# Kernel optimization log

Measured on AMD Instinct MI355X. Metric: run time of the kernel, lower is better.

## Reference

```python
import jax, jax.numpy as jnp
import numpy as np

N_NODES = 50000
N_EDGES = 800000
IN_C = 128
OUT_C = 128
ALPHA = 0.2  # leaky_relu negative slope (args.egat_alpha)
EDGE_K = 3   # edgefeat width, fixed by W_out in-dim = 3*out_channels


def setup_inputs() -> dict:
    key = jax.random.key(0)
    k = jax.random.split(key, 7)
    h = jax.random.normal(k[0], (N_NODES, IN_C), dtype=jnp.float32)
    edge_index = jax.random.randint(k[1], (2, N_EDGES), 0, N_NODES, dtype=jnp.int64)
    edgefeat = jax.random.uniform(k[2], (N_EDGES, EDGE_K), dtype=jnp.float32)
    # glorot-initialized linear weights (stored as [in, out] for x @ W)
    def glorot(kk, fan_in, fan_out):
        lim = jnp.sqrt(6.0 / (fan_in + fan_out)).astype(jnp.float32)
        return jax.random.uniform(kk, (fan_in, fan_out), jnp.float32, -lim, lim)
    W = glorot(k[3], IN_C, OUT_C)
    a1 = glorot(k[4], OUT_C, 1)
    a2 = glorot(k[5], OUT_C, 1)
    W_out = glorot(k[6], EDGE_K * OUT_C, OUT_C)
    return {"h": h, "edge_index": edge_index, "edgefeat": edgefeat,
            "W": W, "a1": a1, "a2": a2, "W_out": W_out}


def reference(h, edge_index, edgefeat, W, a1, a2, W_out):
    src = edge_index[0]  # j: message source
    dst = edge_index[1]  # i: aggregation target
    n = h.shape[0]

    Wh = h @ W                                   # [N, C]
    s1 = Wh @ a1                                 # [N, 1] alpha_j scores
    s2 = Wh @ a2                                 # [N, 1] alpha_i scores

    # edge_update: leaky_relu(alpha_j + alpha_i) * edge_attr, then edge softmax over dst
    e = s1[src] + s2[dst]                        # [E, 1]
    e = jnp.where(e >= 0, e, ALPHA * e)
    alpha = e * edgefeat                         # [E, 3]
    m = jax.ops.segment_max(alpha, dst, num_segments=n)      # [N, 3]
    m = jnp.where(jnp.isfinite(m), m, 0.0)
    ex = jnp.exp(alpha - m[dst])
    denom = jax.ops.segment_sum(ex, dst, num_segments=n)     # [N, 3]
    att = ex / (denom[dst] + 1e-16)              # [E, 3] (dropout p applied at eval -> identity)

    # message: outer product att[E,3] x x_j[E,C] -> [E, 3C] -> W_out -> [E, C]
    x_j = Wh[src]                                # [E, C]
    msg = (att[:, :, None] * x_j[:, None, :]).reshape(att.shape[0], EDGE_K * Wh.shape[1])
    msg = msg @ W_out                            # [E, C]

    # aggregate: sum at destination nodes
    out = jax.ops.segment_sum(msg, dst, num_segments=n)      # [N, C]
    return out
```

## Files before the change

### kernel.cpp

```cpp
#include <hip/hip_runtime.h>
#include <hip/hip_bf16.h>

#define ALPHA 0.2f
typedef unsigned int uint32;
typedef __attribute__((ext_vector_type(8))) short short8;
typedef __attribute__((ext_vector_type(4))) float f32x4;

static __device__ __forceinline__ unsigned short f2bf(float f) {
    unsigned int u = __float_as_uint(f);
    u += 0x7fffu + ((u >> 16) & 1u);
    return (unsigned short)(u >> 16);
}
static __device__ __forceinline__ uint32 pk2bf(float lo, float hi) {
    return (uint32)f2bf(lo) | ((uint32)f2bf(hi) << 16);
}
static __device__ __forceinline__ float bflo(uint32 u) { return __uint_as_float(u << 16); }
static __device__ __forceinline__ float bfhi(uint32 u) { return __uint_as_float(u & 0xffff0000u); }

__global__ __launch_bounds__(256) void k1_hist_prep(const int* __restrict__ ei,
                                                    int* __restrict__ counts,
                                                    int* __restrict__ eslot, int E,
                                                    const float* __restrict__ W,
                                                    const float* __restrict__ Wout,
                                                    const float* __restrict__ a1,
                                                    const float* __restrict__ a2,
                                                    unsigned short* __restrict__ WBT,
                                                    unsigned short* __restrict__ WoutT,
                                                    float* __restrict__ w1f,
                                                    float* __restrict__ w2f, int nbh) {
    const int tid = threadIdx.x;
    if ((int)blockIdx.x < nbh) {
        int e = blockIdx.x * 256 + tid;
        if (e < E) eslot[e] = atomicAdd(&counts[ei[E + e]], 1);
        return;
    }
    int bp = blockIdx.x - nbh;
    if (bp < 8) {
        for (int n = bp * 16; n < bp * 16 + 16; ++n)
            for (int c = tid; c < 128; c += 256)
                WBT[n * 128 + c] = f2bf(W[c * 128 + n]);
    } else if (bp < 24) {
        int q = bp - 8;
        for (int n = q * 8; n < q * 8 + 8; ++n)
            for (int c = tid; c < 384; c += 256)
                WoutT[n * 384 + c] = f2bf(Wout[c * 128 + n]);
    } else {
        if (tid < 128) {
            float acc1 = 0.f, acc2 = 0.f;
            for (int c = 0; c < 128; ++c) {
                float w = W[tid * 128 + c];
                acc1 += w * a1[c];
                acc2 += w * a2[c];
            }
            w1f[tid] = acc1;
            w2f[tid] = acc2;
        }
    }
}

__global__ __launch_bounds__(256) void k2_mmy_scan(const float* __restrict__ h,
                                                   const unsigned short* __restrict__ WBT,
                                                   const float* __restrict__ w1f,
                                                   const float* __restrict__ w2f,
                                                   unsigned short* __restrict__ Whb,
                                                   float* __restrict__ s1,
                                                   uint2* __restrict__ PR, int M,
                                                   const int* __restrict__ counts,
                                                   int* __restrict__ rowptr,
                                                   int N, int E, int nbm) {
    __shared__ unsigned short As[64 * 128];
    __shared__ unsigned short Bs[128 * 128];
    __shared__ float ws1[128], ws2[128];
    __shared__ int wsums[4];
    __shared__ int base_s;
    const int tid = threadIdx.x;

    if ((int)blockIdx.x >= nbm) {
        const int bs   = blockIdx.x - nbm;
        const int lane = tid & 63, wv = tid >> 6;
        const int limit = bs * 1024;
        int acc = 0;
        for (int i = tid * 4; i < limit; i += 1024) {
            int4 v = *(const int4*)(counts + i);
            acc += v.x + v.y + v.z + v.w;
        }
#pragma unroll
        for (int off = 32; off > 0; off >>= 1) acc += __shfl_down(acc, off);
        if (lane == 0) wsums[wv] = acc;
        __syncthreads();
        if (tid == 0) base_s = wsums[0] + wsums[1] + wsums[2] + wsums[3];
        __syncthreads();
        int i0 = bs * 1024 + tid * 4;
        int v0 = 0, v1 = 0, v2 = 0, v3 = 0;
        if (i0 + 3 < N) {
            int4 v = *(const int4*)(counts + i0);
            v0 = v.x; v1 = v.y; v2 = v.z; v3 = v.w;
        } else {
            if (i0 + 0 < N) v0 = counts[i0 + 0];
            if (i0 + 1 < N) v1 = counts[i0 + 1];
            if (i0 + 2 < N) v2 = counts[i0 + 2];
            if (i0 + 3 < N) v3 = counts[i0 + 3];
        }
        int tt = v0 + v1 + v2 + v3;
        int incl = tt;
#pragma unroll
        for (int off = 1; off < 64; off <<= 1) {
            int t = __shfl_up(incl, off);
            if (lane >= off) incl += t;
        }
        __syncthreads();
        if (lane == 63) wsums[wv] = incl;
        __syncthreads();
        int woff = 0;
        for (int w2 = 0; w2 < wv; ++w2) woff += wsums[w2];
        int base = base_s + woff + (incl - tt);
        if (i0 + 0 < N) { rowptr[i0 + 0] = base;                PR[i0 + 0].y = (uint32)base; }
        if (i0 + 1 < N) { rowptr[i0 + 1] = base + v0;           PR[i0 + 1].y = (uint32)(base + v0); }
        if (i0 + 2 < N) { rowptr[i0 + 2] = base + v0 + v1;      PR[i0 + 2].y = (uint32)(base + v0 + v1); }
        if (i0 + 3 < N) { rowptr[i0 + 3] = base + v0 + v1 + v2; PR[i0 + 3].y = (uint32)(base + v0 + v1 + v2); }
        if (bs == 0 && tid == 0) rowptr[N] = E;
        return;
    }

    const int lane = tid & 63;
    const int w    = tid >> 6;
    const int row0 = blockIdx.x * 64;

    if (tid < 128) ws1[tid] = w1f[tid];
    else           ws2[tid - 128] = w2f[tid - 128];
    __syncthreads();

    const float4* h4 = (const float4*)h;
    float sp1[4], sp2[4];
#pragma unroll
    for (int m = 0; m < 4; ++m) { sp1[m] = 0.f; sp2[m] = 0.f; }
#pragma unroll
    for (int m = 0; m < 4; ++m) {
        int i = m * 256 + tid;
        int r = i >> 4, g = i & 15;
        int rg = row0 + r;
        float4 va = make_float4(0.f, 0.f, 0.f, 0.f), vb = va;
        if (rg < M) {
            va = h4[(size_t)rg * 32 + g * 2];
            vb = h4[(size_t)rg * 32 + g * 2 + 1];
        }
        float4 wa1 = *(const float4*)(ws1 + g * 8);
        float4 wb1 = *(const float4*)(ws1 + g * 8 + 4);
        float4 wa2 = *(const float4*)(ws2 + g * 8);
        float4 wb2 = *(const float4*)(ws2 + g * 8 + 4);
        sp1[m] += va.x * wa1.x + va.y * wa1.y + va.z * wa1.z + va.w * wa1.w
                + vb.x * wb1.x + vb.y * wb1.y + vb.z * wb1.z + vb.w * wb1.w;
        sp2[m] += va.x * wa2.x + va.y * wa2.y + va.z * wa2.z + va.w * wa2.w
                + vb.x * wb2.x + vb.y * wb2.y + vb.z * wb2.z + vb.w * wb2.w;
        uint4 u;
        u.x = pk2bf(va.x, va.y); u.y = pk2bf(va.z, va.w);
        u.z = pk2bf(vb.x, vb.y); u.w = pk2bf(vb.z, vb.w);
        *(uint4*)(As + r * 128 + ((g ^ (r & 15)) * 8)) = u;
    }
#pragma unroll
    for (int m = 0; m < 4; ++m) {
#pragma unroll
        for (int off = 1; off < 16; off <<= 1) {
            sp1[m] += __shfl_xor(sp1[m], off);
            sp2[m] += __shfl_xor(sp2[m], off);
        }
    }
    if ((tid & 15) == 0) {
#pragma unroll
        for (int m = 0; m < 4; ++m) {
            int rg = row0 + m * 16 + (tid >> 4);
            if (rg < M) { s1[rg] = sp1[m]; PR[rg].x = __float_as_uint(sp2[m]); }
        }
    }

#pragma unroll
    for (int m = 0; m < 8; ++m) {
        int i = m * 256 + tid;
        int n = i >> 4, g = i & 15;
        uint4 v = *(const uint4*)(WBT + n * 128 + g * 8);
        *(uint4*)(Bs + n * 128 + ((g ^ (n & 15)) * 8)) = v;
    }
    __syncthreads();

    const int ml   = lane & 15;
    const int quad = lane >> 4;
    f32x4 acc[8];
#pragma unroll
    for (int nt = 0; nt < 8; ++nt) acc[nt] = (f32x4){0.f, 0.f, 0.f, 0.f};
#pragma unroll
    for (int kc = 0; kc < 4; ++kc) {
        int gl = ((kc * 4 + quad) ^ ml) * 8;
        short8 af = *(const short8*)(As + (w * 16 + ml) * 128 + gl);
#pragma unroll
        for (int nt = 0; nt < 8; ++nt) {
            short8 bf = *(const short8*)(Bs + (nt * 16 + ml) * 128 + gl);
            acc[nt] = __builtin_amdgcn_mfma_f32_16x16x32_bf16(af, bf, acc[nt], 0, 0, 0);
        }
    }
    __syncthreads();
    unsigned short* Ct = Bs;
    int lrow = w * 16 + quad * 4;
#pragma unroll
    for (int r = 0; r < 4; ++r)
#pragma unroll
        for (int nt = 0; nt < 8; ++nt)
            Ct[(lrow + r) * 136 + nt * 16 + ml] = f2bf(acc[nt][r]);
    __syncthreads();
#pragma unroll
    for (int m = 0; m < 4; ++m) {
        int i = m * 256 + tid;
        int r2 = i >> 4, g = i & 15;
        int rg = row0 + r2;
        uint4 v = *(const uint4*)(Ct + r2 * 136 + g * 8);
        if (rg < M)
            *(uint4*)(Whb + (size_t)rg * 128 + g * 8) = v;
    }
}

__global__ __launch_bounds__(256) void scatter_kernel(const int* __restrict__ ei,
                                                      const float* __restrict__ ef,
                                                      const float* __restrict__ s1,
                                                      const uint2* __restrict__ PR,
                                                      const int* __restrict__ eslot,
                                                      uint2* __restrict__ rec8, int E) {
    int e = blockIdx.x * blockDim.x + threadIdx.x;
    if (e >= E) return;
    int src = ei[e];
    int dst = ei[E + e];
    uint2 pr = PR[dst];
    float s = s1[src] + __uint_as_float(pr.x);
    s = (s >= 0.f) ? s : ALPHA * s;
    unsigned short b0 = f2bf(__expf(s * ef[e * 3 + 0]));
    unsigned short b1 = f2bf(__expf(s * ef[e * 3 + 1]));
    unsigned short b2 = f2bf(__expf(s * ef[e * 3 + 2]));
    uint2 rv;
    rv.x = (uint32)src | ((uint32)(b0 & 0x7fffu) << 17);
    rv.y = (uint32)(b1 & 0x7fffu) | ((uint32)(b2 & 0x7fffu) << 15);
    int pos = (int)pr.y + eslot[e];
    rec8[pos] = rv;
}

__global__ __launch_bounds__(1024) void agg_fused(const uint2* __restrict__ rec8,
                                                  const int* __restrict__ rowptr,
                                                  const uint32* __restrict__ Yu,
                                                  const unsigned short* __restrict__ WoutT,
                                                  float* __restrict__ out, int N) {
    __shared__ float CtS[2 * 16 * 132];
    uint32* zs32 = (uint32*)CtS;
    const int tid  = threadIdx.x;
    const int lane = tid & 63, w = tid >> 6;
    const int ml   = lane & 15, quad = lane >> 4;
    const int nb   = blockIdx.x * 16;
    const int node = nb + w;

    if (node < N) {
        int beg = rowptr[node], end = rowptr[node + 1];

        float d0 = 0.f, d1 = 0.f, d2 = 0.f;
        float z0l = 0.f, z0h = 0.f, z1l = 0.f, z1h = 0.f, z2l = 0.f, z2h = 0.f;
        int j = beg;
        for (; j + 7 < end; j += 8) {
            uint2 rr[8];
#pragma unroll
            for (int q = 0; q < 8; ++q) rr[q] = rec8[j + q];
            uint32 sx[8], sy[8];
#pragma unroll
            for (int q = 0; q < 8; ++q) {
                sx[q] = __builtin_amdgcn_readfirstlane(rr[q].x);
                sy[q] = __builtin_amdgcn_readfirstlane(rr[q].y);
            }
            uint32 u[8];
#pragma unroll
            for (int q = 0; q < 8; ++q)
                u[q] = Yu[(size_t)(sx[q] & 0x1ffffu) * 64 + lane];
#pragma unroll
            for (int q = 0; q < 8; ++q) {
                float w0 = __uint_as_float((sx[q] >> 1) & 0x7fff0000u);
                float w1 = __uint_as_float((sy[q] << 16) & 0x7fff0000u);
                float w2 = __uint_as_float((sy[q] << 1) & 0x7fff0000u);
                d0 += w0; d1 += w1; d2 += w2;
                float yl = bflo(u[q]), yh = bfhi(u[q]);
                z0l += w0 * yl; z0h += w0 * yh;
                z1l += w1 * yl; z1h += w1 * yh;
                z2l += w2 * yl; z2h += w2 * yh;
            }
        }
        for (; j + 3 < end; j += 4) {
            uint2 rr[4];
#pragma unroll
            for (int q = 0; q < 4; ++q) rr[q] = rec8[j + q];
            uint32 sx[4], sy[4];
#pragma unroll
            for (int q = 0; q < 4; ++q) {
                sx[q] = __builtin_amdgcn_readfirstlane(rr[q].x);
                sy[q] = __builtin_amdgcn_readfirstlane(rr[q].y);
            }
            uint32 u[4];
#pragma unroll
            for (int q = 0; q < 4; ++q)
                u[q] = Yu[(size_t)(sx[q] & 0x1ffffu) * 64 + lane];
#pragma unroll
            for (int q = 0; q < 4; ++q) {
                float w0 = __uint_as_float((sx[q] >> 1) & 0x7fff0000u);
                float w1 = __uint_as_float((sy[q] << 16) & 0x7fff0000u);
                float w2 = __uint_as_float((sy[q] << 1) & 0x7fff0000u);
                d0 += w0; d1 += w1; d2 += w2;
                float yl = bflo(u[q]), yh = bfhi(u[q]);
                z0l += w0 * yl; z0h += w0 * yh;
                z1l += w1 * yl; z1h += w1 * yh;
                z2l += w2 * yl; z2h += w2 * yh;
            }
        }
        for (; j < end; ++j) {
            uint2 r0 = rec8[j];
            uint32 sx = __builtin_amdgcn_readfirstlane(r0.x);
            uint32 sy = __builtin_amdgcn_readfirstlane(r0.y);
            uint32 u0 = Yu[(size_t)(sx & 0x1ffffu) * 64 + lane];
            float w0 = __uint_as_float((sx >> 1) & 0x7fff0000u);
            float w1 = __uint_as_float((sy << 16) & 0x7fff0000u);
            float w2 = __uint_as_float((sy << 1) & 0x7fff0000u);
            d0 += w0; d1 += w1; d2 += w2;
            float yl = bflo(u0), yh = bfhi(u0);
            z0l += w0 * yl; z0h += w0 * yh;
            z1l += w1 * yl; z1h += w1 * yh;
            z2l += w2 * yl; z2h += w2 * yh;
        }
        float i0 = 1.f / (d0 + 1e-16f);
        float i1 = 1.f / (d1 + 1e-16f);
        float i2 = 1.f / (d2 + 1e-16f);
        uint32 zp[3] = { pk2bf(z0l * i0, z0h * i0),
                         pk2bf(z1l * i1, z1h * i1),
                         pk2bf(z2l * i2, z2h * i2) };
#pragma unroll
        for (int k = 0; k < 3; ++k) {
            int g  = k * 16 + (lane >> 2);
            int sg = (g & ~7) | ((g ^ w) & 7);
            zs32[w * 192 + sg * 4 + (lane & 3)] = zp[k];
        }
    } else {
#pragma unroll
        for (int k = 0; k < 3; ++k)
            zs32[w * 192 + k * 64 + lane] = 0u;
    }
    __syncthreads();

    const int n0 = (w & 7) * 16;
    const int kh = w >> 3;
    f32x4 acc = (f32x4){0.f, 0.f, 0.f, 0.f};
    const unsigned short* zs16 = (const unsigned short*)zs32;
#pragma unroll
    for (int ks = 0; ks < 6; ++ks) {
        int g  = kh * 24 + ks * 4 + quad;
        int sg = (g & ~7) | ((g ^ ml) & 7);
        short8 af = *(const short8*)(zs16 + ml * 384 + sg * 8);
        short8 bf = *(const short8*)(WoutT + (size_t)(n0 + ml) * 384 + g * 8);
        acc = __builtin_amdgcn_mfma_f32_16x16x32_bf16(af, bf, acc, 0, 0, 0);
    }
    __syncthreads();
#pragma unroll
    for (int r = 0; r < 4; ++r)
        CtS[kh * 2112 + (quad * 4 + r) * 132 + n0 + ml] = acc[r];
    __syncthreads();
    if (tid < 512) {
        int row = tid >> 5, g = tid & 31;
        int nd  = nb + row;
        if (nd < N) {
            float4 a = *(const float4*)(CtS + row * 132 + g * 4);
            float4 b = *(const float4*)(CtS + 2112 + row * 132 + g * 4);
            *(float4*)(out + (size_t)nd * 128 + g * 4) =
                make_float4(a.x + b.x, a.y + b.y, a.z + b.z, a.w + b.w);
        }
    }
}

extern "C" void kernel_launch(void* const* d_in, const int* in_sizes, int n_in,
                              void* d_out, int out_size, void* d_ws, size_t ws_size,
                              hipStream_t stream) {
    const float* h    = (const float*)d_in[0];
    const int*   ei   = (const int*)d_in[1];
    const float* ef   = (const float*)d_in[2];
    const float* W    = (const float*)d_in[3];
    const float* a1   = (const float*)d_in[4];
    const float* a2   = (const float*)d_in[5];
    const float* Wout = (const float*)d_in[6];
    float*       out  = (float*)d_out;

    const int N = in_sizes[0] / 128;
    const int E = in_sizes[2] / 3;
    const int nchunk = (N + 1023) / 1024;
    const int nbh    = (E + 255) / 256;
    const int nbm    = (N + 63) / 64;

    uint2* rec8 = (uint2*)d_ws;
    unsigned short* Whb = (unsigned short*)(rec8 + E);
    unsigned short* WBT = Whb + (size_t)N * 128;
    unsigned short* WoutT = WBT + 128 * 128;
    float* w1f  = (float*)(WoutT + 128 * 384);
    float* w2f  = w1f + 128;
    float* s1   = w2f + 128;
    uint2* PR   = (uint2*)(s1 + N);
    int* rowptr = (int*)(PR + N);
    int* counts = rowptr + N + 4;
    int* eslot  = counts + N;

    (void)hipMemsetAsync(counts, 0, (size_t)N * sizeof(int), stream);

    k1_hist_prep<<<nbh + 25, 256, 0, stream>>>(ei, counts, eslot, E,
                                               W, Wout, a1, a2, WBT, WoutT, w1f, w2f, nbh);
    k2_mmy_scan<<<nbm + nchunk, 256, 0, stream>>>(h, WBT, w1f, w2f, Whb, s1, PR, N,
                                                  counts, rowptr, N, E, nbm);
    scatter_kernel<<<(E + 255) / 256, 256, 0, stream>>>(ei, ef, s1, PR, eslot, rec8, E);
    agg_fused<<<(N + 15) / 16, 1024, 0, stream>>>(rec8, rowptr, (const uint32*)Whb,
                                                  WoutT, out, N);
}
```

Baseline: 238.1 us.

## Balance edge work across warps in a block via edge-range split and LDS atomics

Instead of one wavefront per destination node, the block's combined edge range for its 16 nodes is split evenly across the 16 wavefronts. Each wavefront accumulates partial sums and flushes them into a shared-memory float buffer with atomic adds whenever it crosses a row boundary. Normalization and bf16 packing then read from that buffer. This targets load imbalance from nodes with varying degree, at the cost of LDS atomics, extra zero-initialization, and per-edge row-boundary checks.

New measurement: 405.2 us. 70.2% more time.

```diff
diff --git a/kernel.cpp b/kernel.cpp
--- a/kernel.cpp
+++ b/kernel.cpp
@@ -245,21 +245,59 @@
                                                   const uint32* __restrict__ Yu,
                                                   const unsigned short* __restrict__ WoutT,
                                                   float* __restrict__ out, int N) {
-    __shared__ float CtS[2 * 16 * 132];
-    uint32* zs32 = (uint32*)CtS;
+    __shared__ float zf[16][390];
+    __shared__ uint32 zs32[16 * 192];
+    __shared__ int rp[17];
     const int tid  = threadIdx.x;
     const int lane = tid & 63, w = tid >> 6;
     const int ml   = lane & 15, quad = lane >> 4;
     const int nb   = blockIdx.x * 16;
-    const int node = nb + w;
-
-    if (node < N) {
-        int beg = rowptr[node], end = rowptr[node + 1];
-
-        float d0 = 0.f, d1 = 0.f, d2 = 0.f;
+
+    for (int i = tid; i < 16 * 390; i += 1024) (&zf[0][0])[i] = 0.f;
+    if (tid < 17) rp[tid] = rowptr[min(nb + tid, N)];
+    __syncthreads();
+
+    const int beg = rp[0], end = rp[16];
+    const int chunk = (end - beg + 15) >> 4;
+    int j    = beg + w * chunk;
+    int jEnd = min(j + chunk, end);
+
+    if (j < jEnd) {
+        int r = 0;
+        while (r < 15 && rp[r + 1] <= j) ++r;
         float z0l = 0.f, z0h = 0.f, z1l = 0.f, z1h = 0.f, z2l = 0.f, z2h = 0.f;
-        int j = beg;
-        for (; j + 7 < end; j += 8) {
+        float dd0 = 0.f, dd1 = 0.f, dd2 = 0.f;
+
+#define FLUSH_ROW()                                                         \
+        do {                                                                \
+            atomicAdd(&zf[r][lane * 2],       z0l);                         \
+            atomicAdd(&zf[r][lane * 2 + 1],   z0h);                         \
+            atomicAdd(&zf[r][128 + lane * 2], z1l);                         \
+            atomicAdd(&zf[r][129 + lane * 2], z1h);                         \
+            atomicAdd(&zf[r][256 + lane * 2], z2l);                         \
+            atomicAdd(&zf[r][257 + lane * 2], z2h);                         \
+            if (lane == 0) {                                                \
+                atomicAdd(&zf[r][384], dd0);                                \
+                atomicAdd(&zf[r][385], dd1);                                \
+                atomicAdd(&zf[r][386], dd2);                                \
+            }                                                               \
+            z0l = z0h = z1l = z1h = z2l = z2h = 0.f;                        \
+            dd0 = dd1 = dd2 = 0.f;                                          \
+        } while (0)
+
+#define EDGE_BODY(SX, SY, U)                                                \
+        do {                                                                \
+            float w0 = __uint_as_float(((SX) >> 1) & 0x7fff0000u);          \
+            float w1 = __uint_as_float(((SY) << 16) & 0x7fff0000u);         \
+            float w2 = __uint_as_float(((SY) << 1) & 0x7fff0000u);          \
+            dd0 += w0; dd1 += w1; dd2 += w2;                                \
+            float yl = bflo(U), yh = bfhi(U);                               \
+            z0l += w0 * yl; z0h += w0 * yh;                                 \
+            z1l += w1 * yl; z1h += w1 * yh;                                 \
+            z2l += w2 * yl; z2h += w2 * yh;                                 \
+        } while (0)
+
+        for (; j + 7 < jEnd; j += 8) {
             uint2 rr[8];
 #pragma unroll
             for (int q = 0; q < 8; ++q) rr[q] = rec8[j + q];
@@ -275,72 +313,37 @@
                 u[q] = Yu[(size_t)(sx[q] & 0x1ffffu) * 64 + lane];
 #pragma unroll
             for (int q = 0; q < 8; ++q) {
-                float w0 = __uint_as_float((sx[q] >> 1) & 0x7fff0000u);
-                float w1 = __uint_as_float((sy[q] << 16) & 0x7fff0000u);
-                float w2 = __uint_as_float((sy[q] << 1) & 0x7fff0000u);
-                d0 += w0; d1 += w1; d2 += w2;
-                float yl = bflo(u[q]), yh = bfhi(u[q]);
-                z0l += w0 * yl; z0h += w0 * yh;
-                z1l += w1 * yl; z1h += w1 * yh;
-                z2l += w2 * yl; z2h += w2 * yh;
+                while (j + q >= rp[r + 1]) { FLUSH_ROW(); ++r; }
+                EDGE_BODY(sx[q], sy[q], u[q]);
             }
         }
-        for (; j + 3 < end; j += 4) {
-            uint2 rr[4];
-#pragma unroll
-            for (int q = 0; q < 4; ++q) rr[q] = rec8[j + q];
-            uint32 sx[4], sy[4];
-#pragma unroll
-            for (int q = 0; q < 4; ++q) {
-                sx[q] = __builtin_amdgcn_readfirstlane(rr[q].x);
-                sy[q] = __builtin_amdgcn_readfirstlane(rr[q].y);
-            }
-            uint32 u[4];
-#pragma unroll
-            for (int q = 0; q < 4; ++q)
-                u[q] = Yu[(size_t)(sx[q] & 0x1ffffu) * 64 + lane];
-#pragma unroll
-            for (int q = 0; q < 4; ++q) {
-                float w0 = __uint_as_float((sx[q] >> 1) & 0x7fff0000u);
-                float w1 = __uint_as_float((sy[q] << 16) & 0x7fff0000u);
-                float w2 = __uint_as_float((sy[q] << 1) & 0x7fff0000u);
-                d0 += w0; d1 += w1; d2 += w2;
-                float yl = bflo(u[q]), yh = bfhi(u[q]);
-                z0l += w0 * yl; z0h += w0 * yh;
-                z1l += w1 * yl; z1h += w1 * yh;
-                z2l += w2 * yl; z2h += w2 * yh;
-            }
-        }
-        for (; j < end; ++j) {
-            uint2 r0 = rec8[j];
-            uint32 sx = __builtin_amdgcn_readfirstlane(r0.x);
-            uint32 sy = __builtin_amdgcn_readfirstlane(r0.y);
+        for (; j < jEnd; ++j) {
+            uint2 rr = rec8[j];
+            uint32 sx = __builtin_amdgcn_readfirstlane(rr.x);
+            uint32 sy = __builtin_amdgcn_readfirstlane(rr.y);
             uint32 u0 = Yu[(size_t)(sx & 0x1ffffu) * 64 + lane];
-            float w0 = __uint_as_float((sx >> 1) & 0x7fff0000u);
-            float w1 = __uint_as_float((sy << 16) & 0x7fff0000u);
-            float w2 = __uint_as_float((sy << 1) & 0x7fff0000u);
-            d0 += w0; d1 += w1; d2 += w2;
-            float yl = bflo(u0), yh = bfhi(u0);
-            z0l += w0 * yl; z0h += w0 * yh;
-            z1l += w1 * yl; z1h += w1 * yh;
-            z2l += w2 * yl; z2h += w2 * yh;
-        }
-        float i0 = 1.f / (d0 + 1e-16f);
-        float i1 = 1.f / (d1 + 1e-16f);
-        float i2 = 1.f / (d2 + 1e-16f);
-        uint32 zp[3] = { pk2bf(z0l * i0, z0h * i0),
-                         pk2bf(z1l * i1, z1h * i1),
-                         pk2bf(z2l * i2, z2h * i2) };
+            while (j >= rp[r + 1]) { FLUSH_ROW(); ++r; }
+            EDGE_BODY(sx, sy, u0);
+        }
+        FLUSH_ROW();
+#undef FLUSH_ROW
+#undef EDGE_BODY
+    }
+    __syncthreads();
+
+    {
+        float i0 = 1.f / (zf[w][384] + 1e-16f);
+        float i1 = 1.f / (zf[w][385] + 1e-16f);
+        float i2 = 1.f / (zf[w][386] + 1e-16f);
+        uint32 zp[3] = { pk2bf(zf[w][lane * 2] * i0,       zf[w][lane * 2 + 1] * i0),
+                         pk2bf(zf[w][128 + lane * 2] * i1, zf[w][129 + lane * 2] * i1),
+                         pk2bf(zf[w][256 + lane * 2] * i2, zf[w][257 + lane * 2] * i2) };
 #pragma unroll
         for (int k = 0; k < 3; ++k) {
             int g  = k * 16 + (lane >> 2);
             int sg = (g & ~7) | ((g ^ w) & 7);
             zs32[w * 192 + sg * 4 + (lane & 3)] = zp[k];
         }
-    } else {
-#pragma unroll
-        for (int k = 0; k < 3; ++k)
-            zs32[w * 192 + k * 64 + lane] = 0u;
     }
     __syncthreads();
 
@@ -357,6 +360,7 @@
         acc = __builtin_amdgcn_mfma_f32_16x16x32_bf16(af, bf, acc, 0, 0, 0);
     }
     __syncthreads();
+    float* CtS = &zf[0][0];
 #pragma unroll
     for (int r = 0; r < 4; ++r)
         CtS[kh * 2112 + (quad * 4 + r) * 132 + n0 + ml] = acc[r];
```
